# Kernel optimization log

Hardware: AMD Instinct MI355X
Metric: run time of the kernel (lower is better)

## Reference

```python
import jax, jax.numpy as jnp
import numpy as np

SIZE = 128      # reconstruction grid (size x size per axial slice)
ANGLES = 128    # number of projection angles after circular interpolation


def setup_inputs() -> dict:
    key = jax.random.key(0)
    # 16 per-angle feature maps stacked: [nf, B, C, H, W]
    features = jax.random.normal(key, (16, 1, 8, 128, 128), dtype=jnp.float32)
    return {"features": features}


def circle_interpolate(features, angles):
    # torch: cat([f.unsqueeze(2) for f in features] + [features[0].unsqueeze(2)], dim=2)
    # then trilinear interpolate to (angles+1, H, W) with align_corners=True, drop last.
    # H and W are unchanged, so with align_corners=True the trilinear resample is
    # exactly identity along H, W and pure linear interpolation along the angle axis.
    stacked = jnp.concatenate([features, features[:1]], axis=0)  # [nf+1, B, C, H, W]
    d_in = stacked.shape[0]
    d_out = angles + 1
    pos = jnp.arange(d_out, dtype=jnp.float32) * ((d_in - 1) / (d_out - 1))
    i0 = jnp.clip(jnp.floor(pos).astype(jnp.int32), 0, d_in - 1)
    i1 = jnp.clip(i0 + 1, 0, d_in - 1)
    w = (pos - i0.astype(jnp.float32))[:, None, None, None, None]
    out = stacked[i0] * (1.0 - w) + stacked[i1] * w  # [angles+1, B, C, H, W]
    return out[:angles]  # drop the wrapped last angle -> [A, B, C, H, W]


def ramp_filter(proj):
    # Ramp (|f|) filter along the detector-u axis (last axis), FFT based.
    W = proj.shape[-1]
    f = jnp.abs(jnp.fft.fftfreq(W)).astype(jnp.float32)
    return jnp.real(jnp.fft.ifft(jnp.fft.fft(proj, axis=-1) * f, axis=-1)).astype(proj.dtype)


def backproject(filtered, size):
    # filtered: [A, B, C, H, W]; H = detector rows == axial z slices, W = detector u.
    # Parallel-beam circular geometry factorizes over z: 2D backprojection per slice.
    A, B, C, H, W = filtered.shape
    coords = jnp.arange(size, dtype=jnp.float32) - (size - 1) / 2.0
    x = coords[:, None]  # [S, 1]
    y = coords[None, :]  # [1, S]
    thetas = jnp.arange(A, dtype=jnp.float32) * np.float32(np.pi / A)

    def body(acc, inp):
        p, th = inp  # p: [B, C, H, W]
        u = x * jnp.cos(th) + y * jnp.sin(th) + (W - 1) / 2.0  # [S, S] detector coord
        i0 = jnp.floor(u).astype(jnp.int32)
        frac = u - i0.astype(jnp.float32)
        v0 = ((i0 >= 0) & (i0 < W)).astype(p.dtype)
        v1 = ((i0 + 1 >= 0) & (i0 + 1 < W)).astype(p.dtype)
        g0 = p[..., jnp.clip(i0, 0, W - 1)]        # gather -> [B, C, H, S, S]
        g1 = p[..., jnp.clip(i0 + 1, 0, W - 1)]
        val = g0 * ((1.0 - frac) * v0) + g1 * (frac * v1)
        return acc + val, None

    acc0 = jnp.zeros((B, C, H, size, size), dtype=filtered.dtype)
    vol, _ = jax.lax.scan(body, acc0, (filtered, thetas))
    # vol is [B, C, z, x, y]; the torch module's fbp returns [B, C, x, y, z] and then
    # applies permute(0,1,4,2,3) -> [B, C, z, x, y], so vol is already the final layout.
    return vol * jnp.float32(np.pi / A)


def reference(features):
    proj = circle_interpolate(features, ANGLES)   # [A, B, C, H, W]
    filtered = ramp_filter(proj)
    return backproject(filtered, SIZE)            # [B, C, H, SIZE, SIZE]
```

## Files before the change

kernel.cpp:

```cpp
#include <hip/hip_runtime.h>
#include <math.h>

#ifndef M_PI
#define M_PI 3.14159265358979323846
#endif

#define GP     130
#define PAD    27
#define KBIAS  90.5f
#define SMIR   181.0f
#define NSLOT  182
#define RSD    184
#define NROWS  34
#define ISTR   325

__global__ __launch_bounds__(1024, 4)
void fbp_fused(const float* __restrict__ F, float* __restrict__ out) {
    __shared__ __align__(16) unsigned s_rows[NROWS * RSD];
    __shared__ float s_g[16][GP];
    __shared__ float s_h[128];
    __shared__ float s_cs[34];
    __shared__ float s_sn[34];

    float* s_cos = (float*)s_rows;
    float* s_raw = (float*)s_rows + 128;
    float* inbox = (float*)s_rows;

    const int t   = threadIdx.x;
    const int blk = blockIdx.x;
    const int hh  = blk & 127;
    const int c   = blk >> 7;

    const float* Fb = F + (((size_t)c * 128 + hh) * 128);
    #pragma unroll
    for (int e = 0; e < 2; ++e) {
        int idx = t + 1024 * e;
        int s = idx >> 7, m = idx & 127;
        s_raw[s * 129 + m] = Fb[(size_t)s * 131072 + m];
    }
    if (t < 128) s_cos[t] = cosf((float)t * (float)(M_PI / 64.0));
    if (t < 34) {
        float th = (float)t * (float)(M_PI / 128.0);
        s_cs[t] = cosf(th);
        s_sn[t] = sinf(th);
    }
    __syncthreads();

    if (t < 128) {
        float sum = (t & 1) ? -64.f : 64.f;
        #pragma unroll
        for (int j = 1; j <= 63; ++j)
            sum = fmaf(2.f * (float)j, s_cos[(j * t) & 127], sum);
        s_h[t] = sum * (1.f / 16384.f);
    }
    __syncthreads();

    {
        const int s  = t >> 6;
        const int n0 = t & 63;
        float fa[2] = {0.f, 0.f};
        const float* rawr = &s_raw[s * 129];
        for (int m = 0; m < 128; ++m) {
            float rm = rawr[m];
            int hb = (n0 - m) & 127;
            fa[0] = fmaf(rm, s_h[hb], fa[0]);
            fa[1] = fmaf(rm, s_h[(hb + 64) & 127], fa[1]);
        }
        s_g[s][n0]      = fa[0];
        s_g[s][n0 + 64] = fa[1];
    }

    const int   l  = t & 63;
    const int   w  = t >> 6;
    const float yl = (float)l - 63.5f;

    float R[4][4], S[4][4];
    #pragma unroll
    for (int m = 0; m < 4; ++m)
        #pragma unroll
        for (int k = 0; k < 4; ++k) { R[m][k] = 0.f; S[m][k] = 0.f; }

    #pragma unroll 1
    for (int ch = 0; ch < 4; ++ch) {
        __syncthreads();
        {
            const int r_id   = t >> 5;
            const int lane32 = t & 31;
            const int g = r_id >> 2, j = r_id & 3;
            const int a = ch * 8 + g + 1;
            const int row = (j == 0) ? a : (j == 1) ? 64 - a
                          : (j == 2) ? a + 64 : 128 - a;
            const int i0 = row >> 3;
            const int i1 = (i0 + 1) & 15;
            const float w_ = (float)(row & 7) * 0.125f;
            const float hs = (a == 32) ? 0.5f : 1.0f;
            const float* g0r = s_g[i0];
            const float* g1r = s_g[i1];
            unsigned* rr = &s_rows[r_id * RSD];
            #pragma unroll
            for (int qq = 0; qq < 6; ++qq) {
                int p = lane32 + 32 * qq;
                if (p < NSLOT) {
                    int ix = p - PAD;
                    float v0 = 0.f, v1 = 0.f;
                    if ((unsigned)ix < 128u)
                        v0 = fmaf(w_, g1r[ix] - g0r[ix], g0r[ix]);
                    int iy = ix + 1;
                    if ((unsigned)iy < 128u)
                        v1 = fmaf(w_, g1r[iy] - g0r[iy], g0r[iy]);
                    rr[p] = __builtin_bit_cast(unsigned,
                        __builtin_amdgcn_cvt_pkrtz(v0 * hs, v1 * hs));
                }
            }
        }
        if (ch == 0 && t < 64) {
            const int r2 = t >> 5;
            const int lane32 = t & 31;
            const int i0 = (r2 * 64) >> 3;
            const float* g0r = s_g[i0];
            unsigned* rr = &s_rows[(32 + r2) * RSD];
            #pragma unroll
            for (int qq = 0; qq < 6; ++qq) {
                int p = lane32 + 32 * qq;
                if (p < NSLOT) {
                    int ix = p - PAD;
                    float v0 = ((unsigned)ix < 128u) ? g0r[ix] : 0.f;
                    int iy = ix + 1;
                    float v1 = ((unsigned)iy < 128u) ? g0r[iy] : 0.f;
                    rr[p] = __builtin_bit_cast(unsigned,
                        __builtin_amdgcn_cvt_pkrtz(v0, v1));
                }
            }
        }
        __syncthreads();

        #define SAMPLE4(U, RA, RB, SA, SB) do {                               \
            int   ii = (int)(U);                                              \
            float fr = __builtin_amdgcn_fractf(U);                            \
            unsigned wt = __builtin_bit_cast(unsigned,                        \
                __builtin_amdgcn_cvt_pkrtz(1.f - fr, fr));                    \
            const unsigned* pp = rowp + ii;                                   \
            unsigned w0 = pp[0];                                              \
            unsigned w1 = pp[RSD];                                            \
            unsigned w2 = pp[2 * RSD];                                        \
            unsigned w3 = pp[3 * RSD];                                        \
            asm("v_dot2_f32_f16 %0, %1, %2, %0" : "+v"(RA) : "v"(wt), "v"(w0));\
            asm("v_dot2_f32_f16 %0, %1, %2, %0" : "+v"(RB) : "v"(wt), "v"(w2));\
            asm("v_dot2_f32_f16 %0, %1, %2, %0" : "+v"(SA) : "v"(wt), "v"(w3));\
            asm("v_dot2_f32_f16 %0, %1, %2, %0" : "+v"(SB) : "v"(wt), "v"(w1));\
        } while (0)

        #pragma unroll 1
        for (int g = 0; g < 8; ++g) {
            const int a = ch * 8 + g + 1;
            const float cs = s_cs[a];
            const float sn = s_sn[a];
            const float ay = fmaf(yl, sn, KBIAS);
            const float by = fmaf(yl, -cs, KBIAS);
            const unsigned* rowp = &s_rows[(4 * g) * RSD];
            #pragma unroll
            for (int m = 0; m < 4; ++m) {
                const float xr = (float)(w * 4 + m) - 63.5f;
                float uA = fmaf(xr, cs, ay);
                float uB = fmaf(xr, sn, by);
                float uC = SMIR - uA;
                float uD = SMIR - uB;
                SAMPLE4(uA, R[m][0], R[m][1], S[m][0], S[m][3]);
                SAMPLE4(uB, R[m][1], R[m][2], S[m][3], S[m][2]);
                SAMPLE4(uC, R[m][2], R[m][3], S[m][2], S[m][1]);
                SAMPLE4(uD, R[m][3], R[m][0], S[m][1], S[m][0]);
            }
        }

        if (ch == 0) {
            const float by = fmaf(yl, -1.f, KBIAS);
            const unsigned* rowp = &s_rows[32 * RSD];
            #define SAMPLE2(U, RA, RB) do {                                   \
                int   ii = (int)(U);                                          \
                float fr = __builtin_amdgcn_fractf(U);                        \
                unsigned wt = __builtin_bit_cast(unsigned,                    \
                    __builtin_amdgcn_cvt_pkrtz(1.f - fr, fr));                \
                const unsigned* pp = rowp + ii;                               \
                unsigned w0 = pp[0];                                          \
                unsigned w1 = pp[RSD];                                        \
                asm("v_dot2_f32_f16 %0, %1, %2, %0" : "+v"(RA) : "v"(wt), "v"(w0));\
                asm("v_dot2_f32_f16 %0, %1, %2, %0" : "+v"(RB) : "v"(wt), "v"(w1));\
            } while (0)
            #pragma unroll
            for (int m = 0; m < 4; ++m) {
                const float xr = (float)(w * 4 + m) - 63.5f;
                float uA = xr + KBIAS;
                float uB = by;
                float uC = SMIR - uA;
                float uD = SMIR - uB;
                SAMPLE2(uA, R[m][0], R[m][1]);
                SAMPLE2(uB, R[m][1], R[m][2]);
                SAMPLE2(uC, R[m][2], R[m][3]);
                SAMPLE2(uD, R[m][3], R[m][0]);
            }
            #undef SAMPLE2
        }
        #undef SAMPLE4
    }

    #pragma unroll
    for (int k = 0; k < 4; ++k) {
        __syncthreads();
        #pragma unroll
        for (int m = 0; m < 4; ++m)
            inbox[(l >> 2) * ISTR + (w * 4 + m) * 5 + (l & 3)] = S[m][k];
        __syncthreads();
        #pragma unroll
        for (int m = 0; m < 4; ++m)
            R[m][(k + 1) & 3] += inbox[w * ISTR + l * 5 + m];
    }

    float* ob = out + (size_t)blk * 16384;
    const float sc = (float)(M_PI / 128.0);
    #pragma unroll
    for (int m = 0; m < 4; ++m) {
        const int X0 = w * 4 + m;
        ob[X0 * 128 + l]                 = R[m][0] * sc;
        ob[(127 - l) * 128 + X0]         = R[m][1] * sc;
        ob[(127 - X0) * 128 + (127 - l)] = R[m][2] * sc;
        ob[l * 128 + (127 - X0)]         = R[m][3] * sc;
    }
}

extern "C" void kernel_launch(void* const* d_in, const int* in_sizes, int n_in,
                              void* d_out, int out_size, void* d_ws, size_t ws_size,
                              hipStream_t stream) {
    const float* F = (const float*)d_in[0];
    float* out = (float*)d_out;
    fbp_fused<<<1024, 1024, 0, stream>>>(F, out);
}
```

Baseline: 333.5 us.

## Precompute all angle rows once with interleaved 4-row layout and fma_mix sampling

Builds all 32 angle-group sample tables in shared memory once, instead of rebuilding them in four chunks separated by barriers. Each detector slot now packs its four symmetric rows as an 8-byte entry, so one sample needs two 64-bit LDS loads rather than four 32-bit loads. The fp16 dot2 with packed weights is replaced by fp32 v_fma_mix instructions, which doubles the FMA count per sample but drops the weight packing. The launch bound also moves to 8 waves per SIMD, and the shared table is about twice as large, which may limit occupancy.

```diff
diff --git a/kernel.cpp b/kernel.cpp
--- a/kernel.cpp
+++ b/kernel.cpp
@@ -9,14 +9,13 @@
 #define PAD    27
 #define KBIAS  90.5f
 #define SMIR   181.0f
-#define NSLOT  182
-#define RSD    184
-#define NROWS  34
+#define NENT   182
+#define GSTR   184
 #define ISTR   325
 
-__global__ __launch_bounds__(1024, 4)
+__global__ __launch_bounds__(1024, 8)
 void fbp_fused(const float* __restrict__ F, float* __restrict__ out) {
-    __shared__ __align__(16) unsigned s_rows[NROWS * RSD];
+    __shared__ __align__(16) unsigned s_rows[32 * GSTR * 2 + GSTR];
     __shared__ float s_g[16][GP];
     __shared__ float s_h[128];
     __shared__ float s_cs[34];
@@ -25,6 +24,7 @@
     float* s_cos = (float*)s_rows;
     float* s_raw = (float*)s_rows + 128;
     float* inbox = (float*)s_rows;
+    unsigned* s_sp = &s_rows[32 * GSTR * 2];
 
     const int t   = threadIdx.x;
     const int blk = blockIdx.x;
@@ -69,6 +69,45 @@
         s_g[s][n0]      = fa[0];
         s_g[s][n0 + 64] = fa[1];
     }
+    __syncthreads();
+
+    {
+        #pragma unroll
+        for (int e = 0; e < 6; ++e) {
+            int task = t + 1024 * e;
+            if (task < 32 * NENT) {
+                int gi = task / NENT;
+                int p  = task - gi * NENT;
+                int a  = gi + 1;
+                const float hs = (a == 32) ? 0.5f : 1.0f;
+                int ix = p - PAD;
+                float v[4];
+                #pragma unroll
+                for (int j = 0; j < 4; ++j) {
+                    int row = (j == 0) ? a : (j == 1) ? 64 - a
+                            : (j == 2) ? 64 + a : 128 - a;
+                    int i0 = row >> 3, i1 = (i0 + 1) & 15;
+                    float w_ = (float)(row & 7) * 0.125f;
+                    float val = 0.f;
+                    if ((unsigned)ix < 128u)
+                        val = fmaf(w_, s_g[i1][ix] - s_g[i0][ix], s_g[i0][ix]) * hs;
+                    v[j] = val;
+                }
+                uint2* slot = (uint2*)&s_rows[(gi * GSTR + p) * 2];
+                uint2 pk;
+                pk.x = __builtin_bit_cast(unsigned, __builtin_amdgcn_cvt_pkrtz(v[0], v[1]));
+                pk.y = __builtin_bit_cast(unsigned, __builtin_amdgcn_cvt_pkrtz(v[2], v[3]));
+                *slot = pk;
+            }
+        }
+        if (t < NENT) {
+            int ix = t - PAD;
+            float v0 = ((unsigned)ix < 128u) ? s_g[0][ix] : 0.f;
+            float v1 = ((unsigned)ix < 128u) ? s_g[8][ix] : 0.f;
+            s_sp[t] = __builtin_bit_cast(unsigned, __builtin_amdgcn_cvt_pkrtz(v0, v1));
+        }
+    }
+    __syncthreads();
 
     const int   l  = t & 63;
     const int   w  = t >> 6;
@@ -80,128 +119,78 @@
         #pragma unroll
         for (int k = 0; k < 4; ++k) { R[m][k] = 0.f; S[m][k] = 0.f; }
 
+    #define MIXLO(ACC, WF, D) \
+        asm("v_fma_mix_f32 %0, %1, %2, %0 op_sel:[0,0,0] op_sel_hi:[0,1,0]" \
+            : "+v"(ACC) : "v"(WF), "v"(D))
+    #define MIXHI(ACC, WF, D) \
+        asm("v_fma_mix_f32 %0, %1, %2, %0 op_sel:[0,1,0] op_sel_hi:[0,1,0]" \
+            : "+v"(ACC) : "v"(WF), "v"(D))
+
+    #define SAMPLE4(U, RA, RB, SA, SB) do {                                   \
+        int   ii  = (int)(U);                                                 \
+        float fr  = __builtin_amdgcn_fractf(U);                               \
+        float omf = 1.f - fr;                                                 \
+        const uint2* pp = (const uint2*)(rowb + ii * 8);                      \
+        uint2 d = pp[0];                                                      \
+        uint2 e = pp[1];                                                      \
+        MIXLO(RA, omf, d.x); MIXLO(RA, fr, e.x);                              \
+        MIXLO(RB, omf, d.y); MIXLO(RB, fr, e.y);                              \
+        MIXHI(SA, omf, d.y); MIXHI(SA, fr, e.y);                              \
+        MIXHI(SB, omf, d.x); MIXHI(SB, fr, e.x);                              \
+    } while (0)
+
     #pragma unroll 1
-    for (int ch = 0; ch < 4; ++ch) {
-        __syncthreads();
-        {
-            const int r_id   = t >> 5;
-            const int lane32 = t & 31;
-            const int g = r_id >> 2, j = r_id & 3;
-            const int a = ch * 8 + g + 1;
-            const int row = (j == 0) ? a : (j == 1) ? 64 - a
-                          : (j == 2) ? a + 64 : 128 - a;
-            const int i0 = row >> 3;
-            const int i1 = (i0 + 1) & 15;
-            const float w_ = (float)(row & 7) * 0.125f;
-            const float hs = (a == 32) ? 0.5f : 1.0f;
-            const float* g0r = s_g[i0];
-            const float* g1r = s_g[i1];
-            unsigned* rr = &s_rows[r_id * RSD];
-            #pragma unroll
-            for (int qq = 0; qq < 6; ++qq) {
-                int p = lane32 + 32 * qq;
-                if (p < NSLOT) {
-                    int ix = p - PAD;
-                    float v0 = 0.f, v1 = 0.f;
-                    if ((unsigned)ix < 128u)
-                        v0 = fmaf(w_, g1r[ix] - g0r[ix], g0r[ix]);
-                    int iy = ix + 1;
-                    if ((unsigned)iy < 128u)
-                        v1 = fmaf(w_, g1r[iy] - g0r[iy], g0r[iy]);
-                    rr[p] = __builtin_bit_cast(unsigned,
-                        __builtin_amdgcn_cvt_pkrtz(v0 * hs, v1 * hs));
-                }
-            }
-        }
-        if (ch == 0 && t < 64) {
-            const int r2 = t >> 5;
-            const int lane32 = t & 31;
-            const int i0 = (r2 * 64) >> 3;
-            const float* g0r = s_g[i0];
-            unsigned* rr = &s_rows[(32 + r2) * RSD];
-            #pragma unroll
-            for (int qq = 0; qq < 6; ++qq) {
-                int p = lane32 + 32 * qq;
-                if (p < NSLOT) {
-                    int ix = p - PAD;
-                    float v0 = ((unsigned)ix < 128u) ? g0r[ix] : 0.f;
-                    int iy = ix + 1;
-                    float v1 = ((unsigned)iy < 128u) ? g0r[iy] : 0.f;
-                    rr[p] = __builtin_bit_cast(unsigned,
-                        __builtin_amdgcn_cvt_pkrtz(v0, v1));
-                }
-            }
-        }
-        __syncthreads();
-
-        #define SAMPLE4(U, RA, RB, SA, SB) do {                               \
-            int   ii = (int)(U);                                              \
-            float fr = __builtin_amdgcn_fractf(U);                            \
-            unsigned wt = __builtin_bit_cast(unsigned,                        \
-                __builtin_amdgcn_cvt_pkrtz(1.f - fr, fr));                    \
-            const unsigned* pp = rowp + ii;                                   \
-            unsigned w0 = pp[0];                                              \
-            unsigned w1 = pp[RSD];                                            \
-            unsigned w2 = pp[2 * RSD];                                        \
-            unsigned w3 = pp[3 * RSD];                                        \
-            asm("v_dot2_f32_f16 %0, %1, %2, %0" : "+v"(RA) : "v"(wt), "v"(w0));\
-            asm("v_dot2_f32_f16 %0, %1, %2, %0" : "+v"(RB) : "v"(wt), "v"(w2));\
-            asm("v_dot2_f32_f16 %0, %1, %2, %0" : "+v"(SA) : "v"(wt), "v"(w3));\
-            asm("v_dot2_f32_f16 %0, %1, %2, %0" : "+v"(SB) : "v"(wt), "v"(w1));\
+    for (int gi = 0; gi < 32; ++gi) {
+        const int a = gi + 1;
+        const float cs = s_cs[a];
+        const float sn = s_sn[a];
+        const float ay = fmaf(yl, sn, KBIAS);
+        const float by = fmaf(yl, -cs, KBIAS);
+        const char* rowb = (const char*)&s_rows[gi * GSTR * 2];
+        #pragma unroll
+        for (int m = 0; m < 4; ++m) {
+            const float xr = (float)(w * 4 + m) - 63.5f;
+            float uA = fmaf(xr, cs, ay);
+            float uB = fmaf(xr, sn, by);
+            float uC = SMIR - uA;
+            float uD = SMIR - uB;
+            SAMPLE4(uA, R[m][0], R[m][1], S[m][0], S[m][3]);
+            SAMPLE4(uB, R[m][1], R[m][2], S[m][3], S[m][2]);
+            SAMPLE4(uC, R[m][2], R[m][3], S[m][2], S[m][1]);
+            SAMPLE4(uD, R[m][3], R[m][0], S[m][1], S[m][0]);
+        }
+    }
+
+    {
+        const float by = fmaf(yl, -1.f, KBIAS);
+        const char* spb = (const char*)s_sp;
+        #define SAMPLE2(U, RA, RB) do {                                       \
+            int   ii  = (int)(U);                                             \
+            float fr  = __builtin_amdgcn_fractf(U);                           \
+            float omf = 1.f - fr;                                             \
+            const unsigned* qq = (const unsigned*)(spb + ii * 4);             \
+            unsigned d0 = qq[0];                                              \
+            unsigned d1 = qq[1];                                              \
+            MIXLO(RA, omf, d0); MIXLO(RA, fr, d1);                            \
+            MIXHI(RB, omf, d0); MIXHI(RB, fr, d1);                            \
         } while (0)
-
-        #pragma unroll 1
-        for (int g = 0; g < 8; ++g) {
-            const int a = ch * 8 + g + 1;
-            const float cs = s_cs[a];
-            const float sn = s_sn[a];
-            const float ay = fmaf(yl, sn, KBIAS);
-            const float by = fmaf(yl, -cs, KBIAS);
-            const unsigned* rowp = &s_rows[(4 * g) * RSD];
-            #pragma unroll
-            for (int m = 0; m < 4; ++m) {
-                const float xr = (float)(w * 4 + m) - 63.5f;
-                float uA = fmaf(xr, cs, ay);
-                float uB = fmaf(xr, sn, by);
-                float uC = SMIR - uA;
-                float uD = SMIR - uB;
-                SAMPLE4(uA, R[m][0], R[m][1], S[m][0], S[m][3]);
-                SAMPLE4(uB, R[m][1], R[m][2], S[m][3], S[m][2]);
-                SAMPLE4(uC, R[m][2], R[m][3], S[m][2], S[m][1]);
-                SAMPLE4(uD, R[m][3], R[m][0], S[m][1], S[m][0]);
-            }
-        }
-
-        if (ch == 0) {
-            const float by = fmaf(yl, -1.f, KBIAS);
-            const unsigned* rowp = &s_rows[32 * RSD];
-            #define SAMPLE2(U, RA, RB) do {                                   \
-                int   ii = (int)(U);                                          \
-                float fr = __builtin_amdgcn_fractf(U);                        \
-                unsigned wt = __builtin_bit_cast(unsigned,                    \
-                    __builtin_amdgcn_cvt_pkrtz(1.f - fr, fr));                \
-                const unsigned* pp = rowp + ii;                               \
-                unsigned w0 = pp[0];                                          \
-                unsigned w1 = pp[RSD];                                        \
-                asm("v_dot2_f32_f16 %0, %1, %2, %0" : "+v"(RA) : "v"(wt), "v"(w0));\
-                asm("v_dot2_f32_f16 %0, %1, %2, %0" : "+v"(RB) : "v"(wt), "v"(w1));\
-            } while (0)
-            #pragma unroll
-            for (int m = 0; m < 4; ++m) {
-                const float xr = (float)(w * 4 + m) - 63.5f;
-                float uA = xr + KBIAS;
-                float uB = by;
-                float uC = SMIR - uA;
-                float uD = SMIR - uB;
-                SAMPLE2(uA, R[m][0], R[m][1]);
-                SAMPLE2(uB, R[m][1], R[m][2]);
-                SAMPLE2(uC, R[m][2], R[m][3]);
-                SAMPLE2(uD, R[m][3], R[m][0]);
-            }
-            #undef SAMPLE2
-        }
-        #undef SAMPLE4
-    }
+        #pragma unroll
+        for (int m = 0; m < 4; ++m) {
+            const float xr = (float)(w * 4 + m) - 63.5f;
+            float uA = xr + KBIAS;
+            float uB = by;
+            float uC = SMIR - uA;
+            float uD = SMIR - uB;
+            SAMPLE2(uA, R[m][0], R[m][1]);
+            SAMPLE2(uB, R[m][1], R[m][2]);
+            SAMPLE2(uC, R[m][2], R[m][3]);
+            SAMPLE2(uD, R[m][3], R[m][0]);
+        }
+        #undef SAMPLE2
+    }
+    #undef SAMPLE4
+    #undef MIXLO
+    #undef MIXHI
 
     #pragma unroll
     for (int k = 0; k < 4; ++k) {
```

After: 281.9 us. 1.18x faster.
